# Performance work log

Hardware: AMD Instinct MI355X
Metric: run time of the kernel (lower is better)

## Reference

```python
import jax, jax.numpy as jnp
import numpy as np

B, S, D, H, E = 2, 512, 768, 12, 8
FF = 4 * D
HD = D // H


def setup_inputs() -> dict:
    key = jax.random.key(0)
    ks = jax.random.split(key, 12)
    s = 0.02
    return {
        "x": jax.random.normal(ks[0], (B, S, D), jnp.float32),
        "ln1_g": jnp.ones((D,), jnp.float32),
        "ln1_b": jnp.zeros((D,), jnp.float32),
        "ln2_g": jnp.ones((D,), jnp.float32),
        "ln2_b": jnp.zeros((D,), jnp.float32),
        "in_proj_w": jax.random.normal(ks[1], (3 * D, D), jnp.float32) * s,
        "in_proj_b": jax.random.normal(ks[2], (3 * D,), jnp.float32) * s,
        "out_proj_w": jax.random.normal(ks[3], (D, D), jnp.float32) * s,
        "out_proj_b": jax.random.normal(ks[4], (D,), jnp.float32) * s,
        "router_w": jax.random.normal(ks[5], (E, D), jnp.float32) * s,
        "router_b": jax.random.normal(ks[6], (E,), jnp.float32) * s,
        "w1": jax.random.normal(ks[7], (E, D, FF), jnp.float32) * s,
        "b1": jax.random.normal(ks[8], (E, FF), jnp.float32) * s,
        "w2": jax.random.normal(ks[9], (E, FF, D), jnp.float32) * s,
        "b2": jax.random.normal(ks[10], (E, D), jnp.float32) * s,
    }


def _layernorm(x, g, b, eps=1e-5):
    mu = x.mean(-1, keepdims=True)
    var = ((x - mu) ** 2).mean(-1, keepdims=True)
    return (x - mu) * jax.lax.rsqrt(var + eps) * g + b


def _forward(x, ln1_g, ln1_b, ln2_g, ln2_b, in_proj_w, in_proj_b,
             out_proj_w, out_proj_b, router_w, router_b, w1, b1, w2, b2):
    # --- self-attention sublayer (pre-norm per torch module ordering) ---
    h = _layernorm(x, ln1_g, ln1_b)
    qkv = h @ in_proj_w.T + in_proj_b                     # [B,S,3D]
    q, k, v = jnp.split(qkv, 3, axis=-1)
    to_heads = lambda t: t.reshape(B, S, H, HD).transpose(0, 2, 1, 3)  # [B,H,S,hd]
    q, k, v = to_heads(q), to_heads(k), to_heads(v)
    scores = jnp.einsum('bhqd,bhkd->bhqk', q, k) / np.float32(np.sqrt(HD))
    attn = jax.nn.softmax(scores, axis=-1)
    o = jnp.einsum('bhqk,bhkd->bhqd', attn, v).transpose(0, 2, 1, 3).reshape(B, S, D)
    o = o @ out_proj_w.T + out_proj_b
    x = x + o
    # --- MoE sublayer: top-2 routing, renormalized gates ---
    h2 = _layernorm(x, ln2_g, ln2_b)
    t = h2.reshape(-1, D)                                  # [T,D]
    logits = t @ router_w.T + router_b                     # [T,E]
    probs = jax.nn.softmax(logits, axis=-1)
    top_v, top_i = jax.lax.top_k(probs, 2)                 # [T,2]
    top_v = top_v / top_v.sum(-1, keepdims=True)
    # per-(token, expert) combine weight (0 if expert not in token's top-2)
    comb = jnp.sum(jax.nn.one_hot(top_i, E, dtype=probs.dtype) * top_v[..., None], axis=1)  # [T,E]
    # dense grouped-FFN: every token through every expert, zero-weighted combine
    hid = jax.nn.gelu(jnp.einsum('td,edf->tef', t, w1) + b1, approximate=False)  # exact GELU as torch
    y = jnp.einsum('tef,efd->ted', hid, w2) + b2           # [T,E,D]
    moe = jnp.einsum('te,ted->td', comb, y).reshape(B, S, D)
    return x + moe


def reference(x, ln1_g, ln1_b, ln2_g, ln2_b, in_proj_w, in_proj_b,
              out_proj_w, out_proj_b, router_w, router_b, w1, b1, w2, b2):
    return _forward(x, ln1_g, ln1_b, ln2_g, ln2_b, in_proj_w, in_proj_b,
                    out_proj_w, out_proj_b, router_w, router_b, w1, b1, w2, b2)
```

## Files before the change

### kernel.cpp

```cpp
#include <hip/hip_runtime.h>
#include <hip/hip_bf16.h>

#define BATCH 2
#define SEQ 512
#define DIM 768
#define HEADS 12
#define NEXP 8
#define FFDIM 3072
#define HDIM 64
#define NTOK (BATCH*SEQ)
#define NENT (2*NTOK)

typedef __hip_bfloat16 bf16;
typedef __attribute__((ext_vector_type(8))) short s8v;
typedef __attribute__((ext_vector_type(4))) float f4v;

typedef __attribute__((address_space(1))) const unsigned char gas_u8;
typedef __attribute__((address_space(3))) unsigned char las_u8;
__device__ __forceinline__ void gload16(const void* g, void* l) {
    __builtin_amdgcn_global_load_lds((gas_u8*)g, (las_u8*)l, 16, 0, 0);
}

__global__ __launch_bounds__(256) void ln_kernel(const float* __restrict__ x,
                                                 const float* __restrict__ g,
                                                 const float* __restrict__ b,
                                                 float* __restrict__ outf,
                                                 bf16* __restrict__ outb) {
    int t = blockIdx.x;
    const float* xr = x + (long)t * DIM;
    int tid = threadIdx.x;
    float v0 = xr[tid], v1 = xr[tid + 256], v2 = xr[tid + 512];
    float s = v0 + v1 + v2;
    __shared__ float red[4];
    #pragma unroll
    for (int o = 32; o; o >>= 1) s += __shfl_xor(s, o);
    if ((tid & 63) == 0) red[tid >> 6] = s;
    __syncthreads();
    s = red[0] + red[1] + red[2] + red[3];
    float mu = s * (1.f / DIM);
    float d0 = v0 - mu, d1 = v1 - mu, d2 = v2 - mu;
    float q = d0*d0 + d1*d1 + d2*d2;
    __shared__ float red2[4];
    #pragma unroll
    for (int o = 32; o; o >>= 1) q += __shfl_xor(q, o);
    if ((tid & 63) == 0) red2[tid >> 6] = q;
    __syncthreads();
    q = red2[0] + red2[1] + red2[2] + red2[3];
    float rstd = rsqrtf(q * (1.f / DIM) + 1e-5f);
    float o0 = d0 * rstd * g[tid]       + b[tid];
    float o1 = d1 * rstd * g[tid + 256] + b[tid + 256];
    float o2 = d2 * rstd * g[tid + 512] + b[tid + 512];
    if (outf) {
        float* of = outf + (long)t * DIM;
        of[tid] = o0; of[tid + 256] = o1; of[tid + 512] = o2;
    }
    if (outb) {
        bf16* ob = outb + (long)t * DIM;
        ob[tid] = __float2bfloat16(o0);
        ob[tid + 256] = __float2bfloat16(o1);
        ob[tid + 512] = __float2bfloat16(o2);
    }
}

template<int WM, int WN, bool GROUPED, bool GELU, int OUTMODE>
__global__ __launch_bounds__(256) void mfma_gemm(
    const bf16* __restrict__ A, const bf16* __restrict__ B,
    const float* __restrict__ bias, const float* __restrict__ resid,
    void* __restrict__ Cv,
    int M, int N, int K, int lda, int ldb, int ldc,
    int zdiv, int ksplit,
    long a_hi, long a_lo, long b_hi, long b_lo, long c_hi, long c_lo,
    long bias_stride, const int* __restrict__ grp_off, float alpha)
{
    constexpr int BM = 32 * WM, BN = 32 * WN;
    constexpr int ACH = BM * 4;
    constexpr int BCH = BN * 4;

    int z = blockIdx.z;
    int ze = z / ksplit, ks = z % ksplit;
    int kper = K / ksplit;
    long aoff, boff, coff;
    int m_count = M;
    if (GROUPED) {
        int m0 = grp_off[ze], m1 = grp_off[ze + 1];
        m_count = m1 - m0;
        if ((int)blockIdx.y * BM >= m_count) return;
        aoff = (long)m0 * lda;
        coff = (long)m0 * ldc;
        boff = (long)ze * b_hi;
    } else {
        int zh = ze / zdiv, zl = ze % zdiv;
        aoff = zh * a_hi + zl * a_lo;
        boff = zh * b_hi + zl * b_lo;
        coff = zh * c_hi + zl * c_lo;
    }
    const short* Ag = (const short*)(A + aoff);
    const short* Bg = (const short*)(B + boff);
    const float* biasp = bias ? bias + (long)ze * bias_stride : nullptr;
    float* Cf = (float*)Cv + coff;
    bf16*  Cb = (bf16*)Cv + coff;

    __shared__ short As[BM * 32];
    __shared__ short Bs[BN * 32];

    int tid = threadIdx.x;
    int wv = tid >> 6, ln = tid & 63;
    int wr = wv >> 1, wc = wv & 1;
    int fr = ln & 15, fq = ln >> 4;
    int bm = blockIdx.y * BM, bn = blockIdx.x * BN;

    f4v acc[WM][WN] = {};

    for (int k0 = ks * kper; k0 < (ks + 1) * kper; k0 += 32) {
        #pragma unroll
        for (int is = 0; is < ACH / 256; ++is) {
            int c = is * 256 + wv * 64 + ln;
            int m = c >> 2, kq = c & 3;
            gload16(Ag + (long)(bm + m) * lda + k0 + kq * 8,
                    &As[(is * 256 + wv * 64) * 8]);
        }
        if constexpr (ACH % 256) {
            if (tid < ACH % 256) {
                int c = (ACH / 256) * 256 + tid;
                int m = c >> 2, kq = c & 3;
                gload16(Ag + (long)(bm + m) * lda + k0 + kq * 8,
                        &As[((ACH / 256) * 256 + wv * 64) * 8]);
            }
        }
        #pragma unroll
        for (int is = 0; is < BCH / 256; ++is) {
            int c = is * 256 + wv * 64 + ln;
            int m = c >> 2, kq = c & 3;
            gload16(Bg + (long)(bn + m) * ldb + k0 + kq * 8,
                    &Bs[(is * 256 + wv * 64) * 8]);
        }
        if constexpr (BCH % 256) {
            if (tid < BCH % 256) {
                int c = (BCH / 256) * 256 + tid;
                int m = c >> 2, kq = c & 3;
                gload16(Bg + (long)(bn + m) * ldb + k0 + kq * 8,
                        &Bs[((BCH / 256) * 256 + wv * 64) * 8]);
            }
        }
        __syncthreads();
        s8v av[WM], bv[WN];
        #pragma unroll
        for (int i = 0; i < WM; ++i)
            av[i] = *(const s8v*)&As[(wr * (WM * 16) + i * 16 + fr) * 32 + fq * 8];
        #pragma unroll
        for (int j = 0; j < WN; ++j)
            bv[j] = *(const s8v*)&Bs[(wc * (WN * 16) + j * 16 + fr) * 32 + fq * 8];
        #pragma unroll
        for (int i = 0; i < WM; ++i)
            #pragma unroll
            for (int j = 0; j < WN; ++j)
                acc[i][j] = __builtin_amdgcn_mfma_f32_16x16x32_bf16(av[i], bv[j], acc[i][j], 0, 0, 0);
        __syncthreads();
    }

    #pragma unroll
    for (int i = 0; i < WM; ++i) {
        #pragma unroll
        for (int r = 0; r < 4; ++r) {
            int row = bm + wr * (WM * 16) + i * 16 + fq * 4 + r;
            if (GROUPED && row >= m_count) continue;
            #pragma unroll
            for (int j = 0; j < WN; ++j) {
                int col = bn + wc * (WN * 16) + j * 16 + fr;
                if (col < N) {
                    float v = acc[i][j][r] * alpha;
                    if (OUTMODE == 2) {
                        atomicAdd(&Cf[(long)row * ldc + col], v);
                    } else {
                        if (biasp) v += biasp[col];
                        if (GELU) v = 0.5f * v * (1.f + erff(v * 0.70710678118654752f));
                        if (resid) v += resid[(long)row * ldc + col];
                        if (OUTMODE == 1) Cb[(long)row * ldc + col] = __float2bfloat16(v);
                        else              Cf[(long)row * ldc + col] = v;
                    }
                }
            }
        }
    }
}

template<int XT, int YCAP, int KS, bool GELU, int OUTMODE>
__global__ __launch_bounds__(256) void moe_gemm(
    const bf16* __restrict__ A, const bf16* __restrict__ B,
    const float* __restrict__ bias, void* __restrict__ Cv,
    int lda, int ldb, int ldc, int Ktot, long b_hi, long bias_stride,
    const int* __restrict__ grp_off, int N)
{
    int bid = blockIdx.x;
    int e = bid & 7;
    int r = bid >> 3;
    int xt = r % XT; r /= XT;
    int yt = r % YCAP;
    int ks = r / YCAP;
    int m0 = grp_off[e], m1 = grp_off[e + 1];
    int m_count = m1 - m0;
    int bm = yt * 128;
    if (bm >= m_count) return;
    int bn = xt * 64;
    int kper = Ktot / KS;

    const short* Ag = (const short*)A + (long)m0 * lda;
    const short* Bg = (const short*)(B + (long)e * b_hi);
    const float* biasp = bias ? bias + (long)e * bias_stride : nullptr;
    float* Cf = (float*)Cv + (long)m0 * ldc;
    bf16*  Cb = (bf16*)Cv + (long)m0 * ldc;

    __shared__ short As[2][128 * 64];
    __shared__ short Bs[2][64 * 64];

    int tid = threadIdx.x;
    int wv = tid >> 6, ln = tid & 63;
    int wr = wv >> 1, wc = wv & 1;
    int fr = ln & 15, fq = ln >> 4;

    f4v acc[4][2] = {};

    auto stage = [&](int buf, int k0) {
        #pragma unroll
        for (int is = 0; is < 4; ++is) {
            int c = is * 256 + wv * 64 + ln;
            int m = c >> 3, q = c & 7;
            int qg = q ^ (m & 7);
            gload16(Ag + (long)(bm + m) * lda + k0 + qg * 8,
                    &As[buf][(is * 256 + wv * 64) * 8]);
        }
        #pragma unroll
        for (int is = 0; is < 2; ++is) {
            int c = is * 256 + wv * 64 + ln;
            int n = c >> 3, q = c & 7;
            int qg = q ^ (n & 7);
            gload16(Bg + (long)(bn + n) * ldb + k0 + qg * 8,
                    &Bs[buf][(is * 256 + wv * 64) * 8]);
        }
    };

    int kbeg = ks * kper;
    int nit = kper / 64;
    stage(0, kbeg);
    __syncthreads();
    int cur = 0;
    for (int it = 0; it < nit; ++it) {
        if (it + 1 < nit) stage(cur ^ 1, kbeg + (it + 1) * 64);
        #pragma unroll
        for (int ksub = 0; ksub < 2; ++ksub) {
            s8v av[4], bv[2];
            int qg = ksub * 4 + fq;
            #pragma unroll
            for (int i = 0; i < 4; ++i) {
                int row = wr * 64 + i * 16 + fr;
                av[i] = *(const s8v*)&As[cur][row * 64 + (qg ^ (row & 7)) * 8];
            }
            #pragma unroll
            for (int j = 0; j < 2; ++j) {
                int row = wc * 32 + j * 16 + fr;
                bv[j] = *(const s8v*)&Bs[cur][row * 64 + (qg ^ (row & 7)) * 8];
            }
            #pragma unroll
            for (int i = 0; i < 4; ++i)
                #pragma unroll
                for (int j = 0; j < 2; ++j)
                    acc[i][j] = __builtin_amdgcn_mfma_f32_16x16x32_bf16(av[i], bv[j], acc[i][j], 0, 0, 0);
        }
        __syncthreads();
        cur ^= 1;
    }

    #pragma unroll
    for (int i = 0; i < 4; ++i) {
        #pragma unroll
        for (int rr = 0; rr < 4; ++rr) {
            int row = bm + wr * 64 + i * 16 + fq * 4 + rr;
            if (row >= m_count) continue;
            #pragma unroll
            for (int j = 0; j < 2; ++j) {
                int col = bn + wc * 32 + j * 16 + fr;
                float v = acc[i][j][rr];
                if (OUTMODE == 2) {
                    atomicAdd(&Cf[(long)row * ldc + col], v);
                } else {
                    if (biasp) v += biasp[col];
                    if (GELU) v = 0.5f * v * (1.f + erff(v * 0.70710678118654752f));
                    Cb[(long)row * ldc + col] = __float2bfloat16(v);
                }
            }
        }
    }
}

__global__ __launch_bounds__(256) void softmax512(const float* __restrict__ s,
                                                  bf16* __restrict__ attn) {
    long row = blockIdx.x;
    const float* p = s + row * 512;
    int tid = threadIdx.x;
    float a = p[tid], b = p[tid + 256];
    float m = fmaxf(a, b);
    __shared__ float red[4], red2[4];
    #pragma unroll
    for (int o = 32; o; o >>= 1) m = fmaxf(m, __shfl_xor(m, o));
    if ((tid & 63) == 0) red[tid >> 6] = m;
    __syncthreads();
    m = fmaxf(fmaxf(red[0], red[1]), fmaxf(red[2], red[3]));
    float e0 = expf(a - m), e1 = expf(b - m);
    float ssum = e0 + e1;
    #pragma unroll
    for (int o = 32; o; o >>= 1) ssum += __shfl_xor(ssum, o);
    if ((tid & 63) == 0) red2[tid >> 6] = ssum;
    __syncthreads();
    ssum = red2[0] + red2[1] + red2[2] + red2[3];
    float inv = 1.f / ssum;
    bf16* ar = attn + row * 512;
    ar[tid]       = __float2bfloat16(e0 * inv);
    ar[tid + 256] = __float2bfloat16(e1 * inv);
}

__global__ __launch_bounds__(256) void vt_kernel(const bf16* __restrict__ qkvb,
                                                 bf16* __restrict__ vt) {
    int st = blockIdx.x;
    int z = blockIdx.y;
    int b = z / HEADS, h = z % HEADS;
    __shared__ short tile[64][65];
    int t = threadIdx.x;
    int d = t & 63, s0 = t >> 6;
    const short* q = (const short*)qkvb;
    #pragma unroll
    for (int i = 0; i < 16; ++i) {
        int s = st * 64 + s0 + i * 4;
        tile[s0 + i * 4][d] = q[(long)(b * SEQ + s) * 2304 + 2 * DIM + h * HDIM + d];
    }
    __syncthreads();
    short* o = (short*)vt;
    #pragma unroll
    for (int i = 0; i < 16; ++i) {
        int d2 = (t >> 6) + i * 4;
        o[(long)(z * 64 + d2) * 512 + st * 64 + (t & 63)] = tile[t & 63][d2];
    }
}

__global__ __launch_bounds__(256) void wtrans_kernel(const float* __restrict__ in,
                                                     bf16* __restrict__ out,
                                                     int R, int C) {
    int z = blockIdx.z;
    long ibase = (long)z * R * C;
    int rt = blockIdx.y * 64, ct = blockIdx.x * 64;
    __shared__ float tile[64][65];
    int t = threadIdx.x;
    int c = t & 63, r0 = t >> 6;
    #pragma unroll
    for (int i = 0; i < 16; ++i)
        tile[r0 + i * 4][c] = in[ibase + (long)(rt + r0 + i * 4) * C + ct + c];
    __syncthreads();
    #pragma unroll
    for (int i = 0; i < 16; ++i) {
        int cc = r0 + i * 4;
        out[ibase + (long)(ct + cc) * R + rt + c] = __float2bfloat16(tile[c][cc]);
    }
}

__global__ __launch_bounds__(256) void cvt_kernel(const float* __restrict__ in,
                                                  bf16* __restrict__ out, long n) {
    long i = ((long)blockIdx.x * 256 + threadIdx.x) * 4;
    if (i >= n) return;
    float4 v = *(const float4*)(in + i);
    out[i]     = __float2bfloat16(v.x);
    out[i + 1] = __float2bfloat16(v.y);
    out[i + 2] = __float2bfloat16(v.z);
    out[i + 3] = __float2bfloat16(v.w);
}

__global__ __launch_bounds__(64) void router_kernel(const float* __restrict__ t2,
                                                    const float* __restrict__ rw,
                                                    const float* __restrict__ rb,
                                                    int* __restrict__ e_sel,
                                                    float* __restrict__ w_sel) {
    int t = blockIdx.x;
    int lane = threadIdx.x;
    const float* tr = t2 + (long)t * DIM;
    float tv[12];
    #pragma unroll
    for (int i = 0; i < 12; ++i) tv[i] = tr[lane + 64 * i];
    float logits[NEXP];
    #pragma unroll
    for (int e = 0; e < NEXP; ++e) {
        const float* wr = rw + (long)e * DIM;
        float s = 0.f;
        #pragma unroll
        for (int i = 0; i < 12; ++i) s += tv[i] * wr[lane + 64 * i];
        #pragma unroll
        for (int o = 32; o; o >>= 1) s += __shfl_xor(s, o);
        logits[e] = s + rb[e];
    }
    if (lane == 0) {
        int e0 = -1, e1 = -1;
        float l0 = -1e30f, l1 = -1e30f;
        #pragma unroll
        for (int e = 0; e < NEXP; ++e) {
            float l = logits[e];
            if (l > l0) { l1 = l0; e1 = e0; l0 = l; e0 = e; }
            else if (l > l1) { l1 = l; e1 = e; }
        }
        float p1 = expf(l1 - l0);
        float inv = 1.f / (1.f + p1);
        e_sel[t * 2] = e0;  e_sel[t * 2 + 1] = e1;
        w_sel[t * 2] = inv; w_sel[t * 2 + 1] = p1 * inv;
    }
}

__global__ __launch_bounds__(1024) void build_lists(const int* __restrict__ e_sel,
                                                    int* __restrict__ entry_tok,
                                                    int* __restrict__ ent_exp,
                                                    int* __restrict__ pos,
                                                    int* __restrict__ grp_off) {
    __shared__ int cnt[NEXP];
    __shared__ int off[NEXP + 1];
    __shared__ int cur[NEXP];
    int tid = threadIdx.x;
    if (tid < NEXP) cnt[tid] = 0;
    __syncthreads();
    for (int i = tid; i < NENT; i += 1024) atomicAdd(&cnt[e_sel[i]], 1);
    __syncthreads();
    if (tid == 0) {
        off[0] = 0;
        for (int e = 0; e < NEXP; ++e) off[e + 1] = off[e] + cnt[e];
        for (int e = 0; e < NEXP; ++e) cur[e] = off[e];
    }
    __syncthreads();
    for (int i = tid; i < NENT; i += 1024) {
        int e = e_sel[i];
        int p = atomicAdd(&cur[e], 1);
        entry_tok[p] = i >> 1;
        ent_exp[p] = e;
        pos[i] = p;
    }
    if (tid < NEXP + 1) grp_off[tid] = off[tid];
}

__global__ __launch_bounds__(256) void gather_kernel(const bf16* __restrict__ t2b,
                                                     const int* __restrict__ entry_tok,
                                                     bf16* __restrict__ t2g) {
    long i = (long)blockIdx.x * 256 + threadIdx.x;
    if (i >= (long)NENT * 192) return;
    int p = (int)(i / 192), q = (int)(i % 192);
    ((uint2*)t2g)[(long)p * 192 + q] = ((const uint2*)t2b)[(long)entry_tok[p] * 192 + q];
}

__global__ __launch_bounds__(256) void prefill_x1(const float* __restrict__ x,
                                                  const float* __restrict__ out_b,
                                                  float* __restrict__ x1) {
    long i = ((long)blockIdx.x * 256 + threadIdx.x) * 4;
    if (i >= (long)NTOK * DIM) return;
    int d = (int)(i % DIM);
    float4 v = *(const float4*)(x + i);
    v.x += out_b[d]; v.y += out_b[d + 1]; v.z += out_b[d + 2]; v.w += out_b[d + 3];
    *(float4*)(x1 + i) = v;
}

__global__ __launch_bounds__(256) void prefill_ybuf(const float* __restrict__ b2,
                                                    const int* __restrict__ ent_exp,
                                                    float* __restrict__ ybuf) {
    long i = ((long)blockIdx.x * 256 + threadIdx.x) * 4;
    if (i >= (long)NENT * DIM) return;
    int p = (int)(i / DIM), d = (int)(i % DIM);
    *(float4*)(ybuf + i) = *(const float4*)(b2 + (long)ent_exp[p] * DIM + d);
}

__global__ __launch_bounds__(256) void combine_kernel(const float* __restrict__ x1,
                                                      const float* __restrict__ ybuf,
                                                      const int* __restrict__ pos,
                                                      const float* __restrict__ wsel,
                                                      float* __restrict__ out) {
    long i = (long)blockIdx.x * 256 + threadIdx.x;
    if (i >= (long)NTOK * DIM) return;
    int t = (int)(i / DIM), d = (int)(i % DIM);
    float v = x1[i];
    v += wsel[t * 2]     * ybuf[(long)pos[t * 2]     * DIM + d];
    v += wsel[t * 2 + 1] * ybuf[(long)pos[t * 2 + 1] * DIM + d];
    out[i] = v;
}

extern "C" void kernel_launch(void* const* d_in, const int* in_sizes, int n_in,
                              void* d_out, int out_size, void* d_ws, size_t ws_size,
                              hipStream_t stream) {
    const float* x        = (const float*)d_in[0];
    const float* ln1_g    = (const float*)d_in[1];
    const float* ln1_b    = (const float*)d_in[2];
    const float* ln2_g    = (const float*)d_in[3];
    const float* ln2_b    = (const float*)d_in[4];
    const float* in_w     = (const float*)d_in[5];
    const float* in_b     = (const float*)d_in[6];
    const float* out_w    = (const float*)d_in[7];
    const float* out_b    = (const float*)d_in[8];
    const float* router_w = (const float*)d_in[9];
    const float* router_b = (const float*)d_in[10];
    const float* w1       = (const float*)d_in[11];
    const float* b1       = (const float*)d_in[12];
    const float* w2       = (const float*)d_in[13];
    const float* b2       = (const float*)d_in[14];
    float* out = (float*)d_out;

    const long TD = (long)NTOK * DIM;
    char* p = (char*)d_ws;
    size_t off = 0;
    auto alloc = [&](size_t bytes) -> void* {
        void* r = p + off; off += (bytes + 255) & ~(size_t)255; return r;
    };
    bf16*  h_b    = (bf16*)alloc(TD * 2);
    bf16*  in_wb  = (bf16*)alloc(2304L * 768 * 2);
    bf16*  qkv_b  = (bf16*)alloc(1024L * 2304 * 2);
    bf16*  out_wb = (bf16*)alloc(768L * 768 * 2);
    bf16*  vt_b   = (bf16*)alloc((24L * 64 + 64) * 512 * 2);
    bf16*  oat_b  = (bf16*)alloc(TD * 2);
    float* x1     = (float*)alloc(TD * 4);
    float* t2     = (float*)alloc(TD * 4);
    bf16*  t2b    = (bf16*)alloc(TD * 2);
    bf16*  t2g    = (bf16*)alloc((2048L + 256) * 768 * 2);
    bf16*  w1t    = (bf16*)alloc(8L * 3072 * 768 * 2);
    bf16*  w2t    = (bf16*)alloc(8L * 768 * 3072 * 2);
    bf16*  hid    = (bf16*)alloc((2048L + 256) * 3072 * 2);
    float* ybuf   = (float*)alloc(2048L * 768 * 4);
    int*   e_sel     = (int*)alloc(NENT * 4);
    float* w_sel     = (float*)alloc(NENT * 4);
    int*   entry_tok = (int*)alloc(NENT * 4);
    int*   ent_exp   = (int*)alloc(NENT * 4);
    int*   pos       = (int*)alloc(NENT * 4);
    int*   grp_off   = (int*)alloc(64);
    float* scores = (float*)w1t;
    bf16*  attn   = (bf16*)((char*)w1t + 24L * 512 * 512 * 4);

    ln_kernel<<<NTOK, 256, 0, stream>>>(x, ln1_g, ln1_b, nullptr, h_b);
    cvt_kernel<<<1728, 256, 0, stream>>>(in_w, in_wb, 2304L * 768);
    cvt_kernel<<<576, 256, 0, stream>>>(out_w, out_wb, 768L * 768);
    mfma_gemm<2, 2, false, false, 1><<<dim3(36, 16, 1), 256, 0, stream>>>(
        h_b, in_wb, in_b, nullptr, qkv_b,
        NTOK, 3 * DIM, DIM, DIM, DIM, 3 * DIM,
        1, 1, 0, 0, 0, 0, 0, 0, 0, nullptr, 1.f);
    mfma_gemm<2, 4, false, false, 0><<<dim3(4, 8, 24), 256, 0, stream>>>(
        qkv_b, qkv_b + DIM, nullptr, nullptr, scores,
        SEQ, SEQ, HDIM, 3 * DIM, 3 * DIM, SEQ,
        HEADS, 1, (long)SEQ * 3 * DIM, HDIM, (long)SEQ * 3 * DIM, HDIM,
        (long)HEADS * SEQ * SEQ, (long)SEQ * SEQ,
        0, nullptr, 0.125f);
    softmax512<<<24 * SEQ, 256, 0, stream>>>(scores, attn);
    vt_kernel<<<dim3(8, 24), 256, 0, stream>>>(qkv_b, vt_b);
    mfma_gemm<1, 2, false, false, 1><<<dim3(1, 16, 24), 256, 0, stream>>>(
        attn, vt_b, nullptr, nullptr, oat_b,
        SEQ, HDIM, SEQ, SEQ, SEQ, DIM,
        HEADS, 1, (long)HEADS * SEQ * SEQ, (long)SEQ * SEQ,
        (long)HEADS * HDIM * SEQ, (long)HDIM * SEQ,
        (long)SEQ * DIM, HDIM,
        0, nullptr, 1.f);
    prefill_x1<<<768, 256, 0, stream>>>(x, out_b, x1);
    mfma_gemm<2, 2, false, false, 2><<<dim3(12, 16, 2), 256, 0, stream>>>(
        oat_b, out_wb, nullptr, nullptr, x1,
        NTOK, DIM, DIM, DIM, DIM, DIM,
        1, 2, 0, 0, 0, 0, 0, 0, 0, nullptr, 1.f);
    ln_kernel<<<NTOK, 256, 0, stream>>>(x1, ln2_g, ln2_b, t2, t2b);
    router_kernel<<<NTOK, 64, 0, stream>>>(t2, router_w, router_b, e_sel, w_sel);
    build_lists<<<1, 1024, 0, stream>>>(e_sel, entry_tok, ent_exp, pos, grp_off);
    gather_kernel<<<1536, 256, 0, stream>>>(t2b, entry_tok, t2g);
    wtrans_kernel<<<dim3(48, 12, 8), 256, 0, stream>>>(w1, w1t, DIM, FFDIM);
    moe_gemm<48, 16, 1, true, 1><<<8 * 48 * 16, 256, 0, stream>>>(
        t2g, w1t, b1, hid,
        DIM, DIM, FFDIM, DIM, (long)FFDIM * DIM, FFDIM, grp_off, FFDIM);
    wtrans_kernel<<<dim3(12, 48, 8), 256, 0, stream>>>(w2, w2t, FFDIM, DIM);
    prefill_ybuf<<<1536, 256, 0, stream>>>(b2, ent_exp, ybuf);
    moe_gemm<12, 16, 4, false, 2><<<8 * 12 * 16 * 4, 256, 0, stream>>>(
        hid, w2t, nullptr, ybuf,
        FFDIM, FFDIM, DIM, FFDIM, (long)DIM * FFDIM, 0, grp_off, DIM);
    combine_kernel<<<3072, 256, 0, stream>>>(x1, ybuf, pos, w_sel, out);
}
```

Before: 210.5 us.

## Fuse fp32 expert-weight transpose and bf16 conversion into MoE GEMM B-tile staging

Drops the two separate wtrans kernels that transposed and converted the fp32 expert weights w1/w2 to bf16. The MoE GEMM now reads fp32 weights straight from global memory into registers, packs pairs of k values into bf16, and writes them into a swizzled LDS layout, prefetching one tile ahead of the MFMA loop. This removes two launches and a full write and re-read of the converted weight buffers. In exchange each block reads fp32 (twice the bytes), does the conversion in the inner loop, and B tiles no longer go through the async global-to-LDS path. Blocks that share an expert repeat the conversion work.

```diff
diff --git a/kernel.cpp b/kernel.cpp
--- a/kernel.cpp
+++ b/kernel.cpp
@@ -19,6 +19,11 @@
 typedef __attribute__((address_space(3))) unsigned char las_u8;
 __device__ __forceinline__ void gload16(const void* g, void* l) {
     __builtin_amdgcn_global_load_lds((gas_u8*)g, (las_u8*)l, 16, 0, 0);
+}
+
+__device__ __forceinline__ unsigned short bf16bits(float f) {
+    __hip_bfloat16 h = __float2bfloat16(f);
+    return *reinterpret_cast<unsigned short*>(&h);
 }
 
 __global__ __launch_bounds__(256) void ln_kernel(const float* __restrict__ x,
@@ -186,10 +191,10 @@
 
 template<int XT, int YCAP, int KS, bool GELU, int OUTMODE>
 __global__ __launch_bounds__(256) void moe_gemm(
-    const bf16* __restrict__ A, const bf16* __restrict__ B,
+    const bf16* __restrict__ A, const float* __restrict__ B,
     const float* __restrict__ bias, void* __restrict__ Cv,
-    int lda, int ldb, int ldc, int Ktot, long b_hi, long bias_stride,
-    const int* __restrict__ grp_off, int N)
+    int lda, int N, int ldc, int Ktot, long b_hi, long bias_stride,
+    const int* __restrict__ grp_off)
 {
     int bid = blockIdx.x;
     int e = bid & 7;
@@ -205,7 +210,7 @@
     int kper = Ktot / KS;
 
     const short* Ag = (const short*)A + (long)m0 * lda;
-    const short* Bg = (const short*)(B + (long)e * b_hi);
+    const float* Bg = B + (long)e * b_hi;
     const float* biasp = bias ? bias + (long)e * bias_stride : nullptr;
     float* Cf = (float*)Cv + (long)m0 * ldc;
     bf16*  Cb = (bf16*)Cv + (long)m0 * ldc;
@@ -217,10 +222,12 @@
     int wv = tid >> 6, ln = tid & 63;
     int wr = wv >> 1, wc = wv & 1;
     int fr = ln & 15, fq = ln >> 4;
+    int kp = tid & 31;
+    int nb = tid >> 5;
 
     f4v acc[4][2] = {};
 
-    auto stage = [&](int buf, int k0) {
+    auto stageA = [&](int buf, int k0) {
         #pragma unroll
         for (int is = 0; is < 4; ++is) {
             int c = is * 256 + wv * 64 + ln;
@@ -229,23 +236,40 @@
             gload16(Ag + (long)(bm + m) * lda + k0 + qg * 8,
                     &As[buf][(is * 256 + wv * 64) * 8]);
         }
-        #pragma unroll
-        for (int is = 0; is < 2; ++is) {
-            int c = is * 256 + wv * 64 + ln;
-            int n = c >> 3, q = c & 7;
-            int qg = q ^ (n & 7);
-            gload16(Bg + (long)(bn + n) * ldb + k0 + qg * 8,
-                    &Bs[buf][(is * 256 + wv * 64) * 8]);
+    };
+    auto loadB = [&](int k0, float4* br) {
+        const float* p0 = Bg + (long)(k0 + 2 * kp) * N + bn + nb * 8;
+        br[0] = *(const float4*)p0;
+        br[1] = *(const float4*)(p0 + 4);
+        br[2] = *(const float4*)(p0 + N);
+        br[3] = *(const float4*)(p0 + N + 4);
+    };
+    auto writeB = [&](int buf, const float4* br) {
+        const float* f = (const float*)br;
+        #pragma unroll
+        for (int i = 0; i < 8; ++i) {
+            unsigned u = ((unsigned)bf16bits(f[i + 8]) << 16) | bf16bits(f[i]);
+            int n = nb * 8 + i;
+            int byte = n * 128 + ((kp * 4) ^ ((n & 7) << 4));
+            *(unsigned*)((char*)&Bs[buf][0] + byte) = u;
         }
     };
 
     int kbeg = ks * kper;
     int nit = kper / 64;
-    stage(0, kbeg);
+    float4 br[4];
+    loadB(kbeg, br);
+    stageA(0, kbeg);
+    writeB(0, br);
     __syncthreads();
     int cur = 0;
     for (int it = 0; it < nit; ++it) {
-        if (it + 1 < nit) stage(cur ^ 1, kbeg + (it + 1) * 64);
+        float4 br2[4];
+        bool more = (it + 1 < nit);
+        if (more) {
+            loadB(kbeg + (it + 1) * 64, br2);
+            stageA(cur ^ 1, kbeg + (it + 1) * 64);
+        }
         #pragma unroll
         for (int ksub = 0; ksub < 2; ++ksub) {
             s8v av[4], bv[2];
@@ -258,7 +282,8 @@
             #pragma unroll
             for (int j = 0; j < 2; ++j) {
                 int row = wc * 32 + j * 16 + fr;
-                bv[j] = *(const s8v*)&Bs[cur][row * 64 + (qg ^ (row & 7)) * 8];
+                bv[j] = *(const s8v*)((const char*)&Bs[cur][0] +
+                                      row * 128 + ((qg * 16) ^ ((row & 7) << 4)));
             }
             #pragma unroll
             for (int i = 0; i < 4; ++i)
@@ -266,6 +291,7 @@
                 for (int j = 0; j < 2; ++j)
                     acc[i][j] = __builtin_amdgcn_mfma_f32_16x16x32_bf16(av[i], bv[j], acc[i][j], 0, 0, 0);
         }
+        if (more) writeB(cur ^ 1, br2);
         __syncthreads();
         cur ^= 1;
     }
@@ -338,26 +364,6 @@
     for (int i = 0; i < 16; ++i) {
         int d2 = (t >> 6) + i * 4;
         o[(long)(z * 64 + d2) * 512 + st * 64 + (t & 63)] = tile[t & 63][d2];
-    }
-}
-
-__global__ __launch_bounds__(256) void wtrans_kernel(const float* __restrict__ in,
-                                                     bf16* __restrict__ out,
-                                                     int R, int C) {
-    int z = blockIdx.z;
-    long ibase = (long)z * R * C;
-    int rt = blockIdx.y * 64, ct = blockIdx.x * 64;
-    __shared__ float tile[64][65];
-    int t = threadIdx.x;
-    int c = t & 63, r0 = t >> 6;
-    #pragma unroll
-    for (int i = 0; i < 16; ++i)
-        tile[r0 + i * 4][c] = in[ibase + (long)(rt + r0 + i * 4) * C + ct + c];
-    __syncthreads();
-    #pragma unroll
-    for (int i = 0; i < 16; ++i) {
-        int cc = r0 + i * 4;
-        out[ibase + (long)(ct + cc) * R + rt + c] = __float2bfloat16(tile[c][cc]);
     }
 }
 
@@ -518,8 +524,8 @@
     float* t2     = (float*)alloc(TD * 4);
     bf16*  t2b    = (bf16*)alloc(TD * 2);
     bf16*  t2g    = (bf16*)alloc((2048L + 256) * 768 * 2);
-    bf16*  w1t    = (bf16*)alloc(8L * 3072 * 768 * 2);
-    bf16*  w2t    = (bf16*)alloc(8L * 768 * 3072 * 2);
+    float* scores = (float*)alloc(24L * 512 * 512 * 4);
+    bf16*  attn   = (bf16*)alloc(24L * 512 * 512 * 2);
     bf16*  hid    = (bf16*)alloc((2048L + 256) * 3072 * 2);
     float* ybuf   = (float*)alloc(2048L * 768 * 4);
     int*   e_sel     = (int*)alloc(NENT * 4);
@@ -528,8 +534,6 @@
     int*   ent_exp   = (int*)alloc(NENT * 4);
     int*   pos       = (int*)alloc(NENT * 4);
     int*   grp_off   = (int*)alloc(64);
-    float* scores = (float*)w1t;
-    bf16*  attn   = (bf16*)((char*)w1t + 24L * 512 * 512 * 4);
 
     ln_kernel<<<NTOK, 256, 0, stream>>>(x, ln1_g, ln1_b, nullptr, h_b);
     cvt_kernel<<<1728, 256, 0, stream>>>(in_w, in_wb, 2304L * 768);
@@ -562,14 +566,12 @@
     router_kernel<<<NTOK, 64, 0, stream>>>(t2, router_w, router_b, e_sel, w_sel);
     build_lists<<<1, 1024, 0, stream>>>(e_sel, entry_tok, ent_exp, pos, grp_off);
     gather_kernel<<<1536, 256, 0, stream>>>(t2b, entry_tok, t2g);
-    wtrans_kernel<<<dim3(48, 12, 8), 256, 0, stream>>>(w1, w1t, DIM, FFDIM);
     moe_gemm<48, 16, 1, true, 1><<<8 * 48 * 16, 256, 0, stream>>>(
-        t2g, w1t, b1, hid,
-        DIM, DIM, FFDIM, DIM, (long)FFDIM * DIM, FFDIM, grp_off, FFDIM);
-    wtrans_kernel<<<dim3(12, 48, 8), 256, 0, stream>>>(w2, w2t, FFDIM, DIM);
+        t2g, w1, b1, hid,
+        DIM, FFDIM, FFDIM, DIM, (long)DIM * FFDIM, FFDIM, grp_off);
     prefill_ybuf<<<1536, 256, 0, stream>>>(b2, ent_exp, ybuf);
     moe_gemm<12, 16, 4, false, 2><<<8 * 12 * 16 * 4, 256, 0, stream>>>(
-        hid, w2t, nullptr, ybuf,
-        FFDIM, FFDIM, DIM, FFDIM, (long)DIM * FFDIM, 0, grp_off, DIM);
+        hid, w2, nullptr, ybuf,
+        FFDIM, DIM, DIM, FFDIM, (long)FFDIM * DIM, 0, grp_off);
     combine_kernel<<<3072, 256, 0, stream>>>(x1, ybuf, pos, w_sel, out);
 }
```

Result: faster. 204.2 us (-2.9%).
